# Kernel tuning notes

Measured on AMD Instinct MI355X. Metric: run time of the kernel, lower is better.

## Reference

```python
import jax, jax.numpy as jnp
import numpy as np

EPS = 1e-6
MAX_TANH_ARG = 15.0


def setup_inputs() -> dict:
    key = jax.random.key(0)
    k1, k2, k3 = jax.random.split(key, 3)
    B, H, N, D = 2, 16, 2048, 64
    return {
        "q": jax.random.normal(k1, (B, H, N, D), dtype=jnp.float32),
        "k": jax.random.normal(k2, (B, H, N, D), dtype=jnp.float32),
        "v": jax.random.normal(k3, (B, H, N, D), dtype=jnp.float32),
        "c": jnp.ones((1,), dtype=jnp.float32),
        "beta": jnp.ones((1,), dtype=jnp.float32),
    }


def _exp_map(x, sqrt_c):
    # tangent space -> Poincare ball
    norm = jnp.maximum(jnp.linalg.norm(x, axis=-1, keepdims=True), EPS)
    tanh_arg = jnp.minimum(sqrt_c * norm, MAX_TANH_ARG)
    return x * (jnp.tanh(tanh_arg) / (sqrt_c * norm))


def reference(q, k, v, c, beta):
    # q, k, v: [B, H, N, D]; c, beta: [1] positive scalars
    causal, use_exp_map = True, True
    N = q.shape[2]
    c = jnp.maximum(c.astype(jnp.float32), EPS)  # [1]
    sqrt_c = jnp.sqrt(c)
    beta = beta.astype(jnp.float32)

    if use_exp_map:
        q_hyp = _exp_map(q, sqrt_c)
        k_hyp = _exp_map(k, sqrt_c)
    else:
        q_hyp, k_hyp = q, k

    q_n2 = jnp.sum(q_hyp * q_hyp, axis=-1, keepdims=True)          # [B,H,N,1]
    k_n2 = jnp.sum(k_hyp * k_hyp, axis=-1, keepdims=True)          # [B,H,N,1]
    qk = jnp.einsum('bhnd,bhmd->bhnm', q_hyp, k_hyp)               # [B,H,N,N]

    diff_n2 = jnp.maximum(q_n2 - 2.0 * qk + jnp.swapaxes(k_n2, -2, -1), 0.0)
    denom = jnp.maximum((1.0 - c * q_n2) * (1.0 - c * jnp.swapaxes(k_n2, -2, -1)), EPS)
    arg = jnp.maximum(1.0 + 2.0 * c * diff_n2 / denom, 1.0 + EPS)
    dist = jnp.arccosh(arg) / sqrt_c                               # Poincare distance
    scores = -beta * dist                                          # [B,H,N,N]

    if causal:
        mask = jnp.triu(jnp.ones((N, N), dtype=bool), k=1)
        scores = jnp.where(mask, -jnp.inf, scores)

    attn = jax.nn.softmax(scores, axis=-1)
    out = jnp.einsum('bhnm,bhmd->bhnd', attn, v)
    return out.astype(q.dtype)
```

## Files before the change

kernel.cpp:

```cpp
#include <hip/hip_runtime.h>
#include <hip/hip_bf16.h>

typedef __bf16 bf16x8 __attribute__((ext_vector_type(8)));
typedef float  f32x4  __attribute__((ext_vector_type(4)));

#define BDIM  2
#define HDIM  16
#define NDIM  2048
#define DDIM  64
#define BH    (BDIM*HDIM)
#define EPSF  1e-6f

#define QK_BLOCKS (BH * NDIM / 16)
#define V_BLOCKS  (BH * NDIM / 64)

__device__ __forceinline__ unsigned short f2bf(float x){
    union { float f; unsigned u; } a; a.f = x;
    unsigned r = a.u + 0x7fffu + ((a.u >> 16) & 1u);
    return (unsigned short)(r >> 16);
}

__global__ __launch_bounds__(256)
void prep(const float* __restrict__ q, const float* __restrict__ k,
          const float* __restrict__ v,
          unsigned short* __restrict__ qh, unsigned short* __restrict__ kh,
          unsigned short* __restrict__ vt,
          float* __restrict__ qn2, float* __restrict__ kn2,
          const float* __restrict__ cp)
{
    __shared__ float t[64][65];
    const int tid = threadIdx.x;

    if (blockIdx.x < QK_BLOCKS){
        const int row = blockIdx.x * 16 + (tid >> 4);
        const int c0  = (tid & 15) * 4;
        const float c   = fmaxf(cp[0], EPSF);
        const float sqc = sqrtf(c);

        {
            float4 x = *(const float4*)(q + (size_t)row * DDIM + c0);
            float ss = fmaf(x.x, x.x, fmaf(x.y, x.y, fmaf(x.z, x.z, x.w * x.w)));
            #pragma unroll
            for (int off = 1; off < 16; off <<= 1) ss += __shfl_xor(ss, off);
            float sn    = fmaxf(sqrtf(ss), EPSF);
            float targ  = fminf(sqc * sn, 15.0f);
            float e     = exp2f(targ * 2.885390082f);
            float th    = (e - 1.0f) * __builtin_amdgcn_rcpf(e + 1.0f);
            float scale = th * __builtin_amdgcn_rcpf(sqc * sn);
            ushort4 o;
            o.x = f2bf(x.x * scale); o.y = f2bf(x.y * scale);
            o.z = f2bf(x.z * scale); o.w = f2bf(x.w * scale);
            *(ushort4*)(qh + (size_t)row * DDIM + c0) = o;
            if ((tid & 15) == 0) qn2[row] = ss * scale * scale;
        }
        {
            float4 x = *(const float4*)(k + (size_t)row * DDIM + c0);
            float ss = fmaf(x.x, x.x, fmaf(x.y, x.y, fmaf(x.z, x.z, x.w * x.w)));
            #pragma unroll
            for (int off = 1; off < 16; off <<= 1) ss += __shfl_xor(ss, off);
            float sn    = fmaxf(sqrtf(ss), EPSF);
            float targ  = fminf(sqc * sn, 15.0f);
            float e     = exp2f(targ * 2.885390082f);
            float th    = (e - 1.0f) * __builtin_amdgcn_rcpf(e + 1.0f);
            float scale = th * __builtin_amdgcn_rcpf(sqc * sn);
            ushort4 o;
            o.x = f2bf(x.x * scale); o.y = f2bf(x.y * scale);
            o.z = f2bf(x.z * scale); o.w = f2bf(x.w * scale);
            *(ushort4*)(kh + (size_t)row * DDIM + c0) = o;
            if ((tid & 15) == 0) kn2[row] = ss * scale * scale;
        }
    } else {
        const int b  = blockIdx.x - QK_BLOCKS;
        const int bh = b >> 5;
        const int n0 = (b & 31) * 64;

        #pragma unroll
        for (int i = 0; i < 4; ++i){
            int ch  = tid + i * 256;
            int row = ch >> 4;
            int c4  = ch & 15;
            const float4 g = *(const float4*)(v + ((size_t)bh * NDIM + n0 + row) * DDIM + c4 * 4);
            t[row][c4*4 + 0] = g.x; t[row][c4*4 + 1] = g.y;
            t[row][c4*4 + 2] = g.z; t[row][c4*4 + 3] = g.w;
        }
        __syncthreads();
        #pragma unroll
        for (int i = 0; i < 4; ++i){
            int ch = tid + i * 256;
            int d  = ch >> 4;
            int nc = ch & 15;
            ushort4 o;
            o.x = f2bf(t[nc*4 + 0][d]); o.y = f2bf(t[nc*4 + 1][d]);
            o.z = f2bf(t[nc*4 + 2][d]); o.w = f2bf(t[nc*4 + 3][d]);
            *(ushort4*)(vt + ((size_t)bh * DDIM + d) * NDIM + n0 + nc * 4) = o;
        }
    }
}

__global__ __launch_bounds__(128, 5)
void hyp_attn(const unsigned short* __restrict__ qh, const unsigned short* __restrict__ kh,
              const unsigned short* __restrict__ vtg,
              const float* __restrict__ qn2g, const float* __restrict__ kn2g,
              const float* __restrict__ cp, const float* __restrict__ bp,
              float* __restrict__ out)
{
    __shared__ unsigned short pw_s[2][16 * 72];

    const int bh  = blockIdx.x;
    const int g   = blockIdx.y;
    const int wid = threadIdx.x >> 6;
    const int t   = 31 - (g >> 1);
    const int j   = 4 * t + 2 * (g & 1) + wid;
    const int l   = threadIdx.x & 63;
    const int l15 = l & 15;
    const int lg  = l >> 4;

    const float c   = fmaxf(cp[0], EPSF);
    const float sqc = sqrtf(c);
    const float nb2 = -bp[0] / sqc;
    const float tc  = 2.0f * c;

    const unsigned short* khb  = kh  + (size_t)bh * (NDIM * DDIM);
    const unsigned short* vtb  = vtg + (size_t)bh * (NDIM * DDIM);
    const float*          kn2b = kn2g + (size_t)bh * NDIM;

    bf16x8 vones;
    #pragma unroll
    for (int i = 0; i < 8; ++i) vones[i] = (__bf16)1.0f;

    const int q0 = j * 16;
    const size_t qbase = ((size_t)bh * NDIM + (q0 + l15)) * DDIM;
    const bf16x8 qa0 = *(const bf16x8*)(qh + qbase + lg * 8);
    const bf16x8 qa1 = *(const bf16x8*)(qh + qbase + 32 + lg * 8);

    const int qr0 = q0 + lg * 4;
    float qn2r[4], omq[4];
    #pragma unroll
    for (int r = 0; r < 4; ++r){
        qn2r[r] = qn2g[(size_t)bh * NDIM + qr0 + r];
        omq[r]  = 1.0f - c * qn2r[r];
    }

    f32x4 O[4], Ls;
    Ls = (f32x4){0.f, 0.f, 0.f, 0.f};
    #pragma unroll
    for (int vd = 0; vd < 4; ++vd) O[vd] = (f32x4){0.f, 0.f, 0.f, 0.f};

    unsigned short* pw = pw_s[wid];
    const int ktend = t;

    for (int kt = 0; kt <= ktend; ++kt){
        const int k0 = kt * 64;

        bf16x8 kf0[4], kf1[4];
        float  kn2m[4];
        #pragma unroll
        for (int f = 0; f < 4; ++f){
            const unsigned short* kp = khb + (size_t)(k0 + f * 16 + l15) * DDIM + lg * 8;
            kf0[f]  = *(const bf16x8*)(kp);
            kf1[f]  = *(const bf16x8*)(kp + 32);
            kn2m[f] = kn2b[k0 + f * 16 + l15];
        }

        f32x4 S[4];
        #pragma unroll
        for (int f = 0; f < 4; ++f){
            f32x4 acc = (f32x4){0.f, 0.f, 0.f, 0.f};
            acc = __builtin_amdgcn_mfma_f32_16x16x32_bf16(qa0, kf0[f], acc, 0, 0, 0);
            acc = __builtin_amdgcn_mfma_f32_16x16x32_bf16(qa1, kf1[f], acc, 0, 0, 0);
            S[f] = acc;
        }

        bf16x8 vf[2][4];
        #pragma unroll
        for (int mc = 0; mc < 2; ++mc)
            #pragma unroll
            for (int vd = 0; vd < 4; ++vd)
                vf[mc][vd] = *(const bf16x8*)(vtb + (size_t)(vd * 16 + l15) * NDIM
                                              + k0 + mc * 32 + lg * 8);

        #pragma unroll
        for (int f = 0; f < 4; ++f){
            const float kn2v = kn2m[f];
            const float omk  = 1.0f - c * kn2v;
            #pragma unroll
            for (int r = 0; r < 4; ++r){
                float diff = fmaf(-2.0f, S[f][r], qn2r[r] + kn2v);
                float den  = fmaxf(omq[r] * omk, EPSF);
                float arg  = fmaxf(fmaf(tc * diff, __builtin_amdgcn_rcpf(den), 1.0f), 1.0f + EPSF);
                float w    = arg + sqrtf(fmaf(arg, arg, -1.0f));
                S[f][r]    = nb2 * __log2f(w);
            }
        }
        if (kt == ktend){
            #pragma unroll
            for (int f = 0; f < 4; ++f){
                const int m = k0 + f * 16 + l15;
                #pragma unroll
                for (int r = 0; r < 4; ++r)
                    if (m > qr0 + r) S[f][r] = -1e30f;
            }
        }

        #pragma unroll
        for (int f = 0; f < 4; ++f){
            const int fx = ((f ^ lg) << 4) + l15;
            #pragma unroll
            for (int r = 0; r < 4; ++r){
                float p = exp2f(S[f][r]);
                pw[(lg * 4 + r) * 72 + fx] = f2bf(p);
            }
        }

        asm volatile("s_waitcnt lgkmcnt(0)" ::: "memory");

        #pragma unroll
        for (int mc = 0; mc < 2; ++mc){
            const int f  = 2 * mc + (lg >> 1);
            const int fx = f ^ ((l15 >> 2) & 3);
            bf16x8 pa = *(const bf16x8*)&pw[l15 * 72 + fx * 16 + (lg & 1) * 8];
            Ls = __builtin_amdgcn_mfma_f32_16x16x32_bf16(pa, vones, Ls, 0, 0, 0);
            #pragma unroll
            for (int vd = 0; vd < 4; ++vd)
                O[vd] = __builtin_amdgcn_mfma_f32_16x16x32_bf16(pa, vf[mc][vd], O[vd], 0, 0, 0);
        }
    }

    #pragma unroll
    for (int r = 0; r < 4; ++r){
        float rl = __builtin_amdgcn_rcpf(fmaxf(Ls[r], 1e-30f));
        #pragma unroll
        for (int vd = 0; vd < 4; ++vd)
            out[((size_t)bh * NDIM + qr0 + r) * DDIM + vd * 16 + l15] = O[vd][r] * rl;
    }
}

extern "C" void kernel_launch(void* const* d_in, const int* in_sizes, int n_in,
                              void* d_out, int out_size, void* d_ws, size_t ws_size,
                              hipStream_t stream)
{
    const float* q   = (const float*)d_in[0];
    const float* k   = (const float*)d_in[1];
    const float* v   = (const float*)d_in[2];
    const float* cp  = (const float*)d_in[3];
    const float* bp  = (const float*)d_in[4];
    float*       out = (float*)d_out;

    char* ws = (char*)d_ws;
    const size_t elems = (size_t)BH * NDIM * DDIM;
    unsigned short* qh  = (unsigned short*)ws;  ws += elems * 2;
    unsigned short* kh  = (unsigned short*)ws;  ws += elems * 2;
    unsigned short* vt  = (unsigned short*)ws;  ws += elems * 2;
    float*          qn2 = (float*)ws;           ws += (size_t)BH * NDIM * 4;
    float*          kn2 = (float*)ws;

    prep<<<QK_BLOCKS + V_BLOCKS, 256, 0, stream>>>(q, k, v, qh, kh, vt, qn2, kn2, cp);
    hyp_attn<<<dim3(BH, 64), 128, 0, stream>>>(qh, kh, vt, qn2, kn2, cp, bp, out);
}
```

Measured before the change: 275.0 us.

## Split causal key loop into chunks with atomic accumulation and separate normalization

The attention kernel gains a third grid dimension that splits each query block's key range into chunks of 8 key tiles. Partial unnormalized outputs and row sums are combined across chunks with global atomic adds, and a new norm_out kernel divides by the summed row weights. This is exact only because the softmax skips max subtraction. The aim is more parallelism and shorter per-block work for long causal rows, which should reduce tail imbalance. The cost is two memsets, atomic traffic on the output, an extra kernel launch, and a lower occupancy hint in launch_bounds.

```diff
diff --git a/kernel.cpp b/kernel.cpp
--- a/kernel.cpp
+++ b/kernel.cpp
@@ -10,6 +10,7 @@
 #define DDIM  64
 #define BH    (BDIM*HDIM)
 #define EPSF  1e-6f
+#define CHUNK 8
 
 #define QK_BLOCKS (BH * NDIM / 16)
 #define V_BLOCKS  (BH * NDIM / 64)
@@ -97,20 +98,25 @@
     }
 }
 
-__global__ __launch_bounds__(128, 5)
+__global__ __launch_bounds__(128, 4)
 void hyp_attn(const unsigned short* __restrict__ qh, const unsigned short* __restrict__ kh,
               const unsigned short* __restrict__ vtg,
               const float* __restrict__ qn2g, const float* __restrict__ kn2g,
               const float* __restrict__ cp, const float* __restrict__ bp,
-              float* __restrict__ out)
+              float* __restrict__ out, float* __restrict__ lsg)
 {
     __shared__ unsigned short pw_s[2][16 * 72];
 
-    const int bh  = blockIdx.x;
-    const int g   = blockIdx.y;
+    const int bh    = blockIdx.x;
+    const int a     = 63 - (int)blockIdx.y;
+    const int chunk = blockIdx.z;
+    const int t     = a >> 1;
+    const int ktbeg = chunk * CHUNK;
+    if (ktbeg > t) return;
+    const int ktlim = min(ktbeg + CHUNK, t + 1);
+
     const int wid = threadIdx.x >> 6;
-    const int t   = 31 - (g >> 1);
-    const int j   = 4 * t + 2 * (g & 1) + wid;
+    const int j   = 2 * a + wid;
     const int l   = threadIdx.x & 63;
     const int l15 = l & 15;
     const int lg  = l >> 4;
@@ -147,9 +153,8 @@
     for (int vd = 0; vd < 4; ++vd) O[vd] = (f32x4){0.f, 0.f, 0.f, 0.f};
 
     unsigned short* pw = pw_s[wid];
-    const int ktend = t;
-
-    for (int kt = 0; kt <= ktend; ++kt){
+
+    for (int kt = ktbeg; kt < ktlim; ++kt){
         const int k0 = kt * 64;
 
         bf16x8 kf0[4], kf1[4];
@@ -192,7 +197,7 @@
                 S[f][r]    = nb2 * __log2f(w);
             }
         }
-        if (kt == ktend){
+        if (kt == t){
             #pragma unroll
             for (int f = 0; f < 4; ++f){
                 const int m = k0 + f * 16 + l15;
@@ -226,13 +231,40 @@
         }
     }
 
-    #pragma unroll
-    for (int r = 0; r < 4; ++r){
-        float rl = __builtin_amdgcn_rcpf(fmaxf(Ls[r], 1e-30f));
-        #pragma unroll
-        for (int vd = 0; vd < 4; ++vd)
-            out[((size_t)bh * NDIM + qr0 + r) * DDIM + vd * 16 + l15] = O[vd][r] * rl;
-    }
+    const int nch = (t >> 3) + 1;
+    if (nch == 1){
+        #pragma unroll
+        for (int r = 0; r < 4; ++r)
+            #pragma unroll
+            for (int vd = 0; vd < 4; ++vd)
+                out[((size_t)bh * NDIM + qr0 + r) * DDIM + vd * 16 + l15] = O[vd][r];
+        if (l15 == 0)
+            #pragma unroll
+            for (int r = 0; r < 4; ++r)
+                lsg[(size_t)bh * NDIM + qr0 + r] = Ls[r];
+    } else {
+        #pragma unroll
+        for (int r = 0; r < 4; ++r)
+            #pragma unroll
+            for (int vd = 0; vd < 4; ++vd)
+                atomicAdd(&out[((size_t)bh * NDIM + qr0 + r) * DDIM + vd * 16 + l15], O[vd][r]);
+        if (l15 == 0)
+            #pragma unroll
+            for (int r = 0; r < 4; ++r)
+                atomicAdd(&lsg[(size_t)bh * NDIM + qr0 + r], Ls[r]);
+    }
+}
+
+__global__ __launch_bounds__(256)
+void norm_out(float* __restrict__ out, const float* __restrict__ lsg)
+{
+    const int idx = blockIdx.x * 256 + threadIdx.x;
+    const int row = idx >> 4;
+    const int c0  = (idx & 15) * 4;
+    const float rl = __builtin_amdgcn_rcpf(fmaxf(lsg[row], 1e-30f));
+    float4 v = *(float4*)(out + (size_t)row * DDIM + c0);
+    v.x *= rl; v.y *= rl; v.z *= rl; v.w *= rl;
+    *(float4*)(out + (size_t)row * DDIM + c0) = v;
 }
 
 extern "C" void kernel_launch(void* const* d_in, const int* in_sizes, int n_in,
@@ -252,8 +284,13 @@
     unsigned short* kh  = (unsigned short*)ws;  ws += elems * 2;
     unsigned short* vt  = (unsigned short*)ws;  ws += elems * 2;
     float*          qn2 = (float*)ws;           ws += (size_t)BH * NDIM * 4;
-    float*          kn2 = (float*)ws;
+    float*          kn2 = (float*)ws;           ws += (size_t)BH * NDIM * 4;
+    float*          lsg = (float*)ws;
+
+    hipMemsetAsync(out, 0, (size_t)out_size * sizeof(float), stream);
+    hipMemsetAsync(lsg, 0, (size_t)BH * NDIM * sizeof(float), stream);
 
     prep<<<QK_BLOCKS + V_BLOCKS, 256, 0, stream>>>(q, k, v, qh, kh, vt, qn2, kn2, cp);
-    hyp_attn<<<dim3(BH, 64), 128, 0, stream>>>(qh, kh, vt, qn2, kn2, cp, bp, out);
-}
+    hyp_attn<<<dim3(BH, 64, 4), 128, 0, stream>>>(qh, kh, vt, qn2, kn2, cp, bp, out, lsg);
+    norm_out<<<(BH * NDIM * DDIM / 4) / 256, 256, 0, stream>>>(out, lsg);
+}
```

New measurement: 244.1 us. 1.13x faster.
